# Performance work log

Hardware: AMD Instinct MI355X
Metric: run time of the kernel (lower is better)

## Reference

```python
import jax, jax.numpy as jnp
import numpy as np

N_QUBITS, Q_DEPTH, N_OUTPUT, BATCH = 8, 6, 8, 16384
_C = np.complex64
_H = (np.array([[1, 1], [1, -1]]) / np.sqrt(2)).astype(_C)
_PX = np.array([[0, 1], [1, 0]], dtype=_C)
_PY = np.array([[0, -1j], [1j, 0]], dtype=_C)
_PZ = np.array([[1, 0], [0, -1]], dtype=_C)

def _swap_rows(n, i, j):
    m = np.eye(n, dtype=_C)
    m[[i, j]] = m[[j, i]]
    return m

_CNOT = _swap_rows(4, 2, 3)          # flip target when control=1
_CZ = np.diag(np.array([1, 1, 1, -1], dtype=_C))
_CSWAP = _swap_rows(8, 5, 6)         # swap |101> <-> |110>
_TOF = _swap_rows(8, 6, 7)           # swap |110> <-> |111>


def _apply(state, U, wires):
    """Apply k-qubit gate U (2^k x 2^k, shared across batch) on given wires.
    state: [B] + [2]*N_QUBITS complex tensor."""
    k = len(wires)
    axes = [w + 1 for w in wires]
    st = jnp.moveaxis(state, axes, list(range(1, k + 1)))
    shp = st.shape
    st = jnp.einsum('ij,bjr->bir', jnp.asarray(U, st.dtype), st.reshape(shp[0], 2 ** k, -1))
    return jnp.moveaxis(st.reshape(shp), list(range(1, k + 1)), axes)


def _apply_batched(state, U, wire):
    """Apply per-sample single-qubit gate U [B,2,2] on `wire`."""
    st = jnp.moveaxis(state, wire + 1, 1)
    shp = st.shape
    st = jnp.einsum('bij,bjr->bir', U, st.reshape(shp[0], 2, -1))
    return jnp.moveaxis(st.reshape(shp), 1, wire + 1)


def _rot_mat(axis, theta):
    """Scalar-angle RX/RY/RZ (axis 0/1/2), PennyLane convention exp(-i theta P / 2)."""
    c = jnp.cos(theta / 2)
    s = jnp.sin(theta / 2)
    z = jnp.zeros_like(c)
    if axis == 0:    # RX
        re = jnp.stack([jnp.stack([c, z]), jnp.stack([z, c])])
        im = jnp.stack([jnp.stack([z, -s]), jnp.stack([-s, z])])
    elif axis == 1:  # RY
        re = jnp.stack([jnp.stack([c, -s]), jnp.stack([s, c])])
        im = jnp.zeros((2, 2), dtype=c.dtype)
    else:            # RZ
        re = jnp.stack([jnp.stack([c, z]), jnp.stack([z, c])])
        im = jnp.stack([jnp.stack([-s, z]), jnp.stack([z, s])])
    return (re.astype(jnp.complex64) + 1j * im.astype(jnp.complex64))


def _ry_batched(theta):
    """Per-sample RY matrices: theta [B] -> [B,2,2] complex64."""
    c = jnp.cos(theta / 2)
    s = jnp.sin(theta / 2)
    U = jnp.stack([jnp.stack([c, -s], -1), jnp.stack([s, c], -1)], -2)
    return U.astype(jnp.complex64)


def _forward(input_features, q_params, d_ry, d_rot, d_g2):
    B = input_features.shape[0]
    n = N_QUBITS
    qw = q_params.reshape(Q_DEPTH, n)
    # |0...0> state, shape [B] + [2]*n
    basis = jnp.zeros((2 ** n,), jnp.complex64).at[0].set(1.0)
    state = (jnp.ones((B, 1), jnp.complex64) * basis[None, :]).reshape((B,) + (2,) * n)
    for w in range(n):
        state = _apply(state, _H, [w])
    two_q = {5: _CNOT, 8: _CZ}
    three_q = {6: _CSWAP, 7: _TOF}
    one_q = {1: _H, 2: _PX, 3: _PY, 4: _PZ}
    for layer in range(Q_DEPTH):
        for node in range(n):
            li, ni = layer % 6, node % 4
            if d_ry[li, ni]:
                state = _apply_batched(state, _ry_batched(input_features[:, node]), node)
            rot = int(d_rot[li, ni])
            if rot < 3:
                state = _apply(state, _rot_mat(rot, qw[layer, node]), [node])
            g2 = int(d_g2[li, ni])
            if g2 in one_q:
                state = _apply(state, one_q[g2], [node])
            elif g2 in two_q:
                state = _apply(state, two_q[g2], [node, (node + 1) % n])
            elif g2 in three_q:
                state = _apply(state, three_q[g2], [node, (node + 1) % n, (node + 2) % n])
    probs = state.real ** 2 + state.imag ** 2  # [B] + [2]*n
    exps = []
    for p in range(N_OUTPUT):
        axes = tuple(i for i in range(1, n + 1) if i != p + 1)
        m = probs.sum(axis=axes)  # [B, 2]
        exps.append(m[:, 0] - m[:, 1])
    return jnp.stack(exps, axis=1)  # [B, N_OUTPUT] float32


def setup_inputs() -> dict:
    key = jax.random.key(0)
    k1, k2, k3, k4, k5 = jax.random.split(key, 5)
    return {
        'input_features': jax.random.normal(k1, (BATCH, N_QUBITS), jnp.float32),
        'q_params': jax.random.normal(k2, (Q_DEPTH * N_QUBITS,), jnp.float32),
        'design_ry': jax.random.randint(k3, (6, 4), 0, 2, jnp.int32),
        'design_rot': jax.random.randint(k4, (6, 4), 0, 4, jnp.int32),
        'design_gate2': jax.random.randint(k5, (6, 4), 0, 9, jnp.int32),
    }


def reference(input_features, q_params, design_ry, design_rot, design_gate2):
    # The circuit design is a static (architecture) choice -> host constants.
    d_ry = np.asarray(design_ry)
    d_rot = np.asarray(design_rot)
    d_g2 = np.asarray(design_gate2)
    return _forward(input_features, q_params, d_ry, d_rot, d_g2)
```

## Files before the change

### kernel.cpp

```cpp
#include <hip/hip_runtime.h>
#include <math.h>

#define NQ 8

#define INV2PI 0.15915494309189535f
__device__ __forceinline__ float fsinr(float th) { return __builtin_amdgcn_sinf(th * INV2PI); }
__device__ __forceinline__ float fcosr(float th) { return __builtin_amdgcn_cosf(th * INV2PI); }

template<int XM>
__device__ __forceinline__ float sx(float v) {
    if constexpr (XM == 0) return v;
    else {
        int r = __builtin_amdgcn_ds_swizzle(__float_as_int(v), (XM << 10) | 0x1F);
        return __int_as_float(r);
    }
}


template<int Q>
__device__ __forceinline__ void realGate(float (&sr)[16], float (&si)[16], int laneq,
                                         float a, float b, float d, float e)
{
    if constexpr (Q < 4) {
        constexpr int M = 1 << Q;
#pragma unroll
        for (int i = 0; i < 16; i++) if (!(i & M)) {
            const int j = i | M;
            float x0r = sr[i], x0i = si[i], x1r = sr[j], x1i = si[j];
            sr[i] = a * x0r + b * x1r;  si[i] = a * x0i + b * x1i;
            sr[j] = d * x0r + e * x1r;  si[j] = d * x0i + e * x1i;
        }
    } else {
        constexpr int XM = 1 << (Q - 4);
        const int bit = (laneq >> (Q - 4)) & 1;
        const float sc = bit ? e : a;
        const float pc = bit ? d : b;
#pragma unroll
        for (int i = 0; i < 16; i++) {
            float pr = sx<XM>(sr[i]);
            float pi = sx<XM>(si[i]);
            sr[i] = sc * sr[i] + pc * pr;
            si[i] = sc * si[i] + pc * pi;
        }
    }
}

template<int Q>
__device__ __forceinline__ void applyRX(float (&sr)[16], float (&si)[16], int laneq,
                                        float c, float s)
{
    if constexpr (Q < 4) {
        constexpr int M = 1 << Q;
#pragma unroll
        for (int i = 0; i < 16; i++) if (!(i & M)) {
            const int j = i | M;
            float x0r = sr[i], x0i = si[i], x1r = sr[j], x1i = si[j];
            sr[i] = c * x0r + s * x1i;  si[i] = c * x0i - s * x1r;
            sr[j] = c * x1r + s * x0i;  si[j] = c * x1i - s * x0r;
        }
    } else {
        constexpr int XM = 1 << (Q - 4);
#pragma unroll
        for (int i = 0; i < 16; i++) {
            float pr = sx<XM>(sr[i]);
            float pi = sx<XM>(si[i]);
            float nr = c * sr[i] + s * pi;
            float ni = c * si[i] - s * pr;
            sr[i] = nr; si[i] = ni;
        }
    }
}

template<int Q>
__device__ __forceinline__ void applyRZ(float (&sr)[16], float (&si)[16], int laneq,
                                        float c, float s)
{
    if constexpr (Q >= 4) {
        const int bit = (laneq >> (Q - 4)) & 1;
        const float t = bit ? -s : s;
#pragma unroll
        for (int i = 0; i < 16; i++) {
            float nr = c * sr[i] + t * si[i];
            float ni = c * si[i] - t * sr[i];
            sr[i] = nr; si[i] = ni;
        }
    } else {
#pragma unroll
        for (int i = 0; i < 16; i++) {
            const float t = ((i >> Q) & 1) ? -s : s;
            float nr = c * sr[i] + t * si[i];
            float ni = c * si[i] - t * sr[i];
            sr[i] = nr; si[i] = ni;
        }
    }
}

template<int Q>
__device__ __forceinline__ void applyZ(float (&sr)[16], float (&si)[16], int laneq)
{
    if constexpr (Q >= 4) {
        const bool f = ((laneq >> (Q - 4)) & 1) != 0;
#pragma unroll
        for (int i = 0; i < 16; i++) {
            sr[i] = f ? -sr[i] : sr[i];
            si[i] = f ? -si[i] : si[i];
        }
    } else {
#pragma unroll
        for (int i = 0; i < 16; i++) if ((i >> Q) & 1) {
            sr[i] = -sr[i]; si[i] = -si[i];
        }
    }
}

__device__ __forceinline__ void swapf(float& a, float& b) { float t = a; a = b; b = t; }

template<int Q>
__device__ __forceinline__ void applyX(float (&sr)[16], float (&si)[16], int laneq)
{
    if constexpr (Q < 4) {
        constexpr int M = 1 << Q;
#pragma unroll
        for (int i = 0; i < 16; i++) if (!(i & M)) {
            swapf(sr[i], sr[i | M]); swapf(si[i], si[i | M]);
        }
    } else {
        constexpr int XM = 1 << (Q - 4);
#pragma unroll
        for (int i = 0; i < 16; i++) {
            sr[i] = sx<XM>(sr[i]);
            si[i] = sx<XM>(si[i]);
        }
    }
}

template<int Q>
__device__ __forceinline__ void applyY(float (&sr)[16], float (&si)[16], int laneq)
{
    if constexpr (Q < 4) {
        constexpr int M = 1 << Q;
#pragma unroll
        for (int i = 0; i < 16; i++) if (!(i & M)) {
            const int j = i | M;
            float x0r = sr[i], x0i = si[i], x1r = sr[j], x1i = si[j];
            sr[i] = x1i;  si[i] = -x1r;
            sr[j] = -x0i; si[j] = x0r;
        }
    } else {
        constexpr int XM = 1 << (Q - 4);
        const int bit = (laneq >> (Q - 4)) & 1;
#pragma unroll
        for (int i = 0; i < 16; i++) {
            float pr = sx<XM>(sr[i]);
            float pi = sx<XM>(si[i]);
            sr[i] = bit ? -pi : pi;
            si[i] = bit ? pr : -pr;
        }
    }
}

template<int C, int T>
__device__ __forceinline__ void applyCZ(float (&sr)[16], float (&si)[16], int laneq)
{
#pragma unroll
    for (int i = 0; i < 16; i++) {
        const int g = i | (laneq << 4);
        const bool f = (((g >> C) & (g >> T)) & 1) != 0;
        sr[i] = f ? -sr[i] : sr[i];
        si[i] = f ? -si[i] : si[i];
    }
}

template<int CM, int M>
__device__ __forceinline__ void applyCPerm(float (&sr)[16], float (&si)[16], int laneq)
{
    constexpr int LX  = M >> 4;
    constexpr int PL  = M & 15;
    constexpr int CML = CM & 15;
    constexpr int CMH = CM >> 4;
    float tr[16], ti[16];
#pragma unroll
    for (int i = 0; i < 16; i++) { tr[i] = sr[i]; ti[i] = si[i]; }
#pragma unroll
    for (int i = 0; i < 16; i++) {
        if ((i & CML) == CML) {
            const int j = i ^ PL;
            float srv = sx<LX>(tr[j]);
            float siv = sx<LX>(ti[j]);
            if constexpr (CMH != 0) {
                const bool c = (laneq & CMH) == CMH;
                sr[i] = c ? srv : sr[i];
                si[i] = c ? siv : si[i];
            } else {
                sr[i] = srv; si[i] = siv;
            }
        }
    }
}

template<int C, int T1, int T2>
__device__ __forceinline__ void applyCSWAP(float (&sr)[16], float (&si)[16], int laneq)
{
    constexpr int M  = (1 << T1) | (1 << T2);
    constexpr int LX = M >> 4;
    constexpr int PL = M & 15;
    float tr[16], ti[16];
#pragma unroll
    for (int i = 0; i < 16; i++) { tr[i] = sr[i]; ti[i] = si[i]; }
#pragma unroll
    for (int i = 0; i < 16; i++) {
        const int g = i | (laneq << 4);
        const bool cnd = (((g >> C) & 1) != 0) && ((((g >> T1) ^ (g >> T2)) & 1) != 0);
        const int j = i ^ PL;
        float srv = sx<LX>(tr[j]);
        float siv = sx<LX>(ti[j]);
        sr[i] = cnd ? srv : sr[i];
        si[i] = cnd ? siv : si[i];
    }
}

template<int N>
__device__ __forceinline__ void nodeStep(float (&sr)[16], float (&si)[16], int laneq,
                                         const float (&fc)[8], const float (&fs)[8],
                                         const float* __restrict__ qp,
                                         const int* __restrict__ dry,
                                         const int* __restrict__ drot,
                                         const int* __restrict__ dg2,
                                         int layer)
{
    constexpr int N1 = (N + 1) & 7;
    constexpr int N2 = (N + 2) & 7;
    const int di = layer * 4 + (N & 3);

    if (dry[di])
        realGate<N>(sr, si, laneq, fc[N], -fs[N], fs[N], fc[N]);

    const int rot = drot[di];
    if (rot < 3) {
        const float th = qp[layer * NQ + N] * 0.5f;
        const float c = fcosr(th), s = fsinr(th);
        if (rot == 0)      applyRX<N>(sr, si, laneq, c, s);
        else if (rot == 1) realGate<N>(sr, si, laneq, c, -s, s, c);
        else               applyRZ<N>(sr, si, laneq, c, s);
    }

    const int g2 = dg2[di];
    switch (g2) {
        case 1: {
            const float r = 0.70710678118654752f;
            realGate<N>(sr, si, laneq, r, r, r, -r);
        } break;
        case 2: applyX<N>(sr, si, laneq); break;
        case 3: applyY<N>(sr, si, laneq); break;
        case 4: applyZ<N>(sr, si, laneq); break;
        case 5: applyCPerm<(1 << N), (1 << N1)>(sr, si, laneq); break;
        case 6: applyCSWAP<N, N1, N2>(sr, si, laneq); break;
        case 7: applyCPerm<(1 << N) | (1 << N1), (1 << N2)>(sr, si, laneq); break;
        case 8: applyCZ<N, N1>(sr, si, laneq); break;
        default: break;
    }
}

__global__ __launch_bounds__(256, 4) void qsim_kernel(
    const float* __restrict__ feats,
    const float* __restrict__ qp,
    const int* __restrict__ dry,
    const int* __restrict__ drot,
    const int* __restrict__ dg2,
    float* __restrict__ out,
    int B)
{
    const int laneq = threadIdx.x & 15;
    const int b     = blockIdx.x * 16 + (threadIdx.x >> 4);
    if (b >= B) return;

    const float4* f4 = (const float4*)(feats + (size_t)b * NQ);
    float4 fA = f4[0], fB = f4[1];
    const float fv[8] = { fA.x, fA.y, fA.z, fA.w, fB.x, fB.y, fB.z, fB.w };
    float fc[8], fs[8];
#pragma unroll
    for (int k = 0; k < 8; k++) {
        fc[k] = fcosr(fv[k] * 0.5f);
        fs[k] = fsinr(fv[k] * 0.5f);
    }

    float sr[16], si[16];
#pragma unroll
    for (int i = 0; i < 16; i++) { sr[i] = 0.0625f; si[i] = 0.0f; }

#pragma unroll 1
    for (int layer = 0; layer < 6; layer++) {
        nodeStep<0>(sr, si, laneq, fc, fs, qp, dry, drot, dg2, layer);
        nodeStep<1>(sr, si, laneq, fc, fs, qp, dry, drot, dg2, layer);
        nodeStep<2>(sr, si, laneq, fc, fs, qp, dry, drot, dg2, layer);
        nodeStep<3>(sr, si, laneq, fc, fs, qp, dry, drot, dg2, layer);
        nodeStep<4>(sr, si, laneq, fc, fs, qp, dry, drot, dg2, layer);
        nodeStep<5>(sr, si, laneq, fc, fs, qp, dry, drot, dg2, layer);
        nodeStep<6>(sr, si, laneq, fc, fs, qp, dry, drot, dg2, layer);
        nodeStep<7>(sr, si, laneq, fc, fs, qp, dry, drot, dg2, layer);
    }

    float p[16];
#pragma unroll
    for (int i = 0; i < 16; i++) p[i] = sr[i] * sr[i] + si[i] * si[i];

    float tot = 0.f;
#pragma unroll
    for (int i = 0; i < 16; i++) tot += p[i];

    float e[4];
#pragma unroll
    for (int q = 0; q < 4; q++) {
        float s0 = 0.f;
#pragma unroll
        for (int i = 0; i < 16; i++) if (!((i >> q) & 1)) s0 += p[i];
        e[q] = 2.f * s0 - tot;
    }

#pragma unroll
    for (int q = 0; q < 4; q++) {
        e[q] += sx<1>(e[q]);
        e[q] += sx<2>(e[q]);
        e[q] += sx<4>(e[q]);
        e[q] += sx<8>(e[q]);
    }
    { float pv = sx<1>(tot); tot = (laneq & 1) ? (pv - tot) : (pv + tot); }
    { float pv = sx<2>(tot); tot = (laneq & 2) ? (pv - tot) : (pv + tot); }
    { float pv = sx<4>(tot); tot = (laneq & 4) ? (pv - tot) : (pv + tot); }
    { float pv = sx<8>(tot); tot = (laneq & 8) ? (pv - tot) : (pv + tot); }

    float* ob = out + (size_t)b * NQ;
    if (laneq == 0)
        *(float4*)ob = make_float4(e[0], e[1], e[2], e[3]);
    if (laneq && !(laneq & (laneq - 1)))
        ob[4 + __builtin_ctz(laneq)] = tot;
}

extern "C" void kernel_launch(void* const* d_in, const int* in_sizes, int n_in,
                              void* d_out, int out_size, void* d_ws, size_t ws_size,
                              hipStream_t stream)
{
    (void)n_in; (void)out_size; (void)d_ws; (void)ws_size;
    const float* feats   = (const float*)d_in[0];
    const float* qparams = (const float*)d_in[1];
    const int* dry       = (const int*)d_in[2];
    const int* drot      = (const int*)d_in[3];
    const int* dg2       = (const int*)d_in[4];
    float* out           = (float*)d_out;

    const int B = in_sizes[0] / NQ;
    const int blocks = (B + 15) / 16;
    qsim_kernel<<<blocks, 256, 0, stream>>>(feats, qparams, dry, drot, dg2, out, B);
}
```

Measured before the change: 127.2 us.

## Specialize controlled-permutation gates to avoid temp copies and cut shuffles

Rewrites the controlled-permutation and controlled-swap gate helpers so each case is handled separately: in-register swaps for intra-thread qubits and direct lane swizzles only where needed, without copying the full state into temporary arrays. This aims to reduce register pressure and the number of cross-lane swizzles and selects. The launch-bounds occupancy hint drops from 4 to 2 blocks per CU, giving the compiler more registers at the cost of fewer resident waves. The final probability reduction is also fused into a single pass.

```diff
diff --git a/kernel.cpp b/kernel.cpp
--- a/kernel.cpp
+++ b/kernel.cpp
@@ -16,6 +16,8 @@
     }
 }
 
+__device__ __forceinline__ void swapf(float& a, float& b) { float t = a; a = b; b = t; }
+
 
 template<int Q>
 __device__ __forceinline__ void realGate(float (&sr)[16], float (&si)[16], int laneq,
@@ -113,8 +115,6 @@
     }
 }
 
-__device__ __forceinline__ void swapf(float& a, float& b) { float t = a; a = b; b = t; }
-
 template<int Q>
 __device__ __forceinline__ void applyX(float (&sr)[16], float (&si)[16], int laneq)
 {
@@ -178,21 +178,34 @@
     constexpr int PL  = M & 15;
     constexpr int CML = CM & 15;
     constexpr int CMH = CM >> 4;
-    float tr[16], ti[16];
-#pragma unroll
-    for (int i = 0; i < 16; i++) { tr[i] = sr[i]; ti[i] = si[i]; }
-#pragma unroll
-    for (int i = 0; i < 16; i++) {
-        if ((i & CML) == CML) {
-            const int j = i ^ PL;
-            float srv = sx<LX>(tr[j]);
-            float siv = sx<LX>(ti[j]);
-            if constexpr (CMH != 0) {
-                const bool c = (laneq & CMH) == CMH;
-                sr[i] = c ? srv : sr[i];
-                si[i] = c ? siv : si[i];
-            } else {
-                sr[i] = srv; si[i] = siv;
+    if constexpr (LX != 0) {
+#pragma unroll
+        for (int i = 0; i < 16; i++) {
+            if ((i & CML) == CML) {
+                float pr = sx<LX>(sr[i]);
+                float pi = sx<LX>(si[i]);
+                if constexpr (CMH != 0) {
+                    const bool c = (laneq & CMH) == CMH;
+                    sr[i] = c ? pr : sr[i];
+                    si[i] = c ? pi : si[i];
+                } else {
+                    sr[i] = pr; si[i] = pi;
+                }
+            }
+        }
+    } else {
+#pragma unroll
+        for (int i = 0; i < 16; i++) {
+            if (!(i & PL) && ((i & CML) == CML)) {
+                const int j = i | PL;
+                if constexpr (CMH != 0) {
+                    const bool c = (laneq & CMH) == CMH;
+                    float t0r = sr[i], t0i = si[i];
+                    sr[i] = c ? sr[j] : sr[i];  si[i] = c ? si[j] : si[i];
+                    sr[j] = c ? t0r : sr[j];    si[j] = c ? t0i : si[j];
+                } else {
+                    swapf(sr[i], sr[j]); swapf(si[i], si[j]);
+                }
             }
         }
     }
@@ -204,18 +217,61 @@
     constexpr int M  = (1 << T1) | (1 << T2);
     constexpr int LX = M >> 4;
     constexpr int PL = M & 15;
-    float tr[16], ti[16];
-#pragma unroll
-    for (int i = 0; i < 16; i++) { tr[i] = sr[i]; ti[i] = si[i]; }
-#pragma unroll
-    for (int i = 0; i < 16; i++) {
-        const int g = i | (laneq << 4);
-        const bool cnd = (((g >> C) & 1) != 0) && ((((g >> T1) ^ (g >> T2)) & 1) != 0);
-        const int j = i ^ PL;
-        float srv = sx<LX>(tr[j]);
-        float siv = sx<LX>(ti[j]);
-        sr[i] = cnd ? srv : sr[i];
-        si[i] = cnd ? siv : si[i];
+
+    if constexpr (LX == 0) {
+#pragma unroll
+        for (int i = 0; i < 16; i++) {
+            if (((i >> T1) & 1) && !((i >> T2) & 1)) {
+                bool skip = false;
+                if constexpr (C < 4) { if (!((i >> C) & 1)) skip = true; }
+                if (!skip) {
+                    const int j = i ^ PL;
+                    if constexpr (C >= 4) {
+                        const bool c = ((laneq >> (C - 4)) & 1) != 0;
+                        float t0r = sr[i], t0i = si[i];
+                        sr[i] = c ? sr[j] : sr[i];  si[i] = c ? si[j] : si[i];
+                        sr[j] = c ? t0r : sr[j];    si[j] = c ? t0i : si[j];
+                    } else {
+                        swapf(sr[i], sr[j]); swapf(si[i], si[j]);
+                    }
+                }
+            }
+        }
+    } else if constexpr (PL == 0) {
+        bool c = ((((laneq >> (T1 - 4)) ^ (laneq >> (T2 - 4))) & 1) != 0);
+        if constexpr (C >= 4) c = c && (((laneq >> (C - 4)) & 1) != 0);
+#pragma unroll
+        for (int i = 0; i < 16; i++) {
+            bool skip = false;
+            if constexpr (C < 4) { if (!((i >> C) & 1)) skip = true; }
+            if (!skip) {
+                float pr = sx<LX>(sr[i]);
+                float pi = sx<LX>(si[i]);
+                sr[i] = c ? pr : sr[i];
+                si[i] = c ? pi : si[i];
+            }
+        }
+    } else {
+        constexpr int TL = (PL == (1 << T1)) ? T2 : T1;
+        const bool laneT = ((laneq >> (TL - 4)) & 1) != 0;
+        bool cc = true;
+        if constexpr (C >= 4) cc = ((laneq >> (C - 4)) & 1) != 0;
+#pragma unroll
+        for (int i = 0; i < 16; i++) {
+            if (!(i & PL)) {
+                bool skip = false;
+                if constexpr (C < 4) { if (!((i >> C) & 1)) skip = true; }
+                if (!skip) {
+                    const int j = i | PL;
+                    float a_r = sx<LX>(sr[j]), a_i = sx<LX>(si[j]);
+                    float b_r = sx<LX>(sr[i]), b_i = sx<LX>(si[i]);
+                    const bool ci = cc && laneT;
+                    const bool cj = cc && !laneT;
+                    sr[i] = ci ? a_r : sr[i];  si[i] = ci ? a_i : si[i];
+                    sr[j] = cj ? b_r : sr[j];  si[j] = cj ? b_i : si[j];
+                }
+            }
+        }
     }
 }
 
@@ -261,7 +317,7 @@
     }
 }
 
-__global__ __launch_bounds__(256, 4) void qsim_kernel(
+__global__ __launch_bounds__(256, 2) void qsim_kernel(
     const float* __restrict__ feats,
     const float* __restrict__ qp,
     const int* __restrict__ dry,
@@ -300,22 +356,17 @@
         nodeStep<7>(sr, si, laneq, fc, fs, qp, dry, drot, dg2, layer);
     }
 
-    float p[16];
-#pragma unroll
-    for (int i = 0; i < 16; i++) p[i] = sr[i] * sr[i] + si[i] * si[i];
-
-    float tot = 0.f;
-#pragma unroll
-    for (int i = 0; i < 16; i++) tot += p[i];
-
-    float e[4];
-#pragma unroll
-    for (int q = 0; q < 4; q++) {
-        float s0 = 0.f;
-#pragma unroll
-        for (int i = 0; i < 16; i++) if (!((i >> q) & 1)) s0 += p[i];
-        e[q] = 2.f * s0 - tot;
-    }
+    float tot = 0.f, s0 = 0.f, s1 = 0.f, s2 = 0.f, s3 = 0.f;
+#pragma unroll
+    for (int i = 0; i < 16; i++) {
+        float p = sr[i] * sr[i] + si[i] * si[i];
+        tot += p;
+        if (!(i & 1)) s0 += p;
+        if (!(i & 2)) s1 += p;
+        if (!(i & 4)) s2 += p;
+        if (!(i & 8)) s3 += p;
+    }
+    float e[4] = { 2.f * s0 - tot, 2.f * s1 - tot, 2.f * s2 - tot, 2.f * s3 - tot };
 
 #pragma unroll
     for (int q = 0; q < 4; q++) {
```

After: 129.3 us. No clear change (+1.7%).
